# Kernel tuning notes

Measured on AMD Instinct MI355X. Metric: run time of the kernel, lower is better.

## Reference

```python
import jax, jax.numpy as jnp
import numpy as np

B, W, I, S, T, U, US = 4, 2000, 64, 64, 24, 32, 2
V, H, D, OUT = 32000, 4, 256, 512
PER = W + I + S + U + 1          # nodes per graph = 2161
N = B * PER                      # 8644 nodes
E_RAND = N * 16


def setup_inputs() -> dict:
    key = jax.random.key(0)
    ks = jax.random.split(key, 24)
    s = 0.02
    inp = {}
    inp["all_words"] = jax.random.randint(ks[0], (B * W,), 0, V)
    inp["image_feats"] = jax.random.normal(ks[1], (B * I, 2048), jnp.float32)
    inp["sentences"] = jax.random.randint(ks[2], (B, S, T), 0, V)
    inp["sentence_mask"] = jnp.ones((B, S, T), jnp.float32)
    inp["utterances"] = jax.random.randint(ks[3], (B, U, US), 0, S)
    inp["utterance_mask"] = jnp.ones((B, U, US), jnp.float32)
    inp["session_ids"] = (jnp.arange(B) + 1) * PER - 1   # last node of each graph
    src = jax.random.randint(ks[4], (E_RAND,), 0, N)
    dst = jax.random.randint(ks[5], (E_RAND,), 0, N)
    loop = jnp.arange(N)
    inp["edge_src"] = jnp.concatenate([src, loop])
    inp["edge_dst"] = jnp.concatenate([dst, loop])
    # learned parameters
    inp["word_embed"] = jax.random.normal(ks[6], (V, 300), jnp.float32) * s
    inp["text_fc_w"] = jax.random.normal(ks[7], (300, 1024), jnp.float32) * s
    inp["text_fc_b"] = jnp.zeros((1024,), jnp.float32)
    inp["image_fc_w"] = jax.random.normal(ks[8], (2048, 1024), jnp.float32) * s
    inp["image_fc_b"] = jnp.zeros((1024,), jnp.float32)
    inp["gat0_fc"] = jax.random.normal(ks[9], (1024, H * D), jnp.float32) * s
    inp["gat0_al"] = jax.random.normal(ks[10], (H, D), jnp.float32) * s
    inp["gat0_ar"] = jax.random.normal(ks[11], (H, D), jnp.float32) * s
    inp["gat0_b"] = jnp.zeros((H * D,), jnp.float32)
    inp["gat1_fc"] = jax.random.normal(ks[12], (H * D, H * D), jnp.float32) * s
    inp["gat1_al"] = jax.random.normal(ks[13], (H, D), jnp.float32) * s
    inp["gat1_ar"] = jax.random.normal(ks[14], (H, D), jnp.float32) * s
    inp["gat1_b"] = jnp.zeros((H * D,), jnp.float32)
    inp["gat2_fc"] = jax.random.normal(ks[15], (H * D, OUT), jnp.float32) * s
    inp["gat2_al"] = jax.random.normal(ks[16], (1, OUT), jnp.float32) * s
    inp["gat2_ar"] = jax.random.normal(ks[17], (1, OUT), jnp.float32) * s
    inp["gat2_b"] = jnp.zeros((OUT,), jnp.float32)
    return inp


def _gat_layer(h, src, dst, fc_w, al, ar, b, act):
    # DGL GATConv: fc -> per-head attention logits -> edge softmax over dst -> aggregate
    n = h.shape[0]
    nh, dd = al.shape
    f = (h @ fc_w).reshape(n, nh, dd)                    # [N,H,D]
    el = (f * al).sum(-1)                                # [N,H]
    er = (f * ar).sum(-1)
    e = jax.nn.leaky_relu(el[src] + er[dst], 0.2)        # [E,H]
    m = jax.ops.segment_max(e, dst, num_segments=n)      # stable softmax per dst node
    a = jnp.exp(e - m[dst])
    z = jax.ops.segment_sum(a, dst, num_segments=n)
    alpha = a / z[dst]                                   # [E,H]
    out = jax.ops.segment_sum(alpha[:, :, None] * f[src], dst, num_segments=n)
    out = out + b.reshape(nh, dd)
    if act:
        out = jax.nn.elu(out)
    return out.reshape(n, nh * dd)


def _masked_mean(x, mask):
    # x: [..., K, F], mask: [..., K]
    s = (x * mask[..., None]).sum(-2)
    cnt = mask.sum(-1, keepdims=True)
    cnt = jnp.where(cnt == 0, 1.0, cnt)
    return s / cnt


def reference(all_words, image_feats, sentences, sentence_mask, utterances,
              utterance_mask, session_ids, edge_src, edge_dst,
              word_embed, text_fc_w, text_fc_b, image_fc_w, image_fc_b,
              gat0_fc, gat0_al, gat0_ar, gat0_b,
              gat1_fc, gat1_al, gat1_ar, gat1_b,
              gat2_fc, gat2_al, gat2_ar, gat2_b):
    b, s_num, t_num = sentences.shape
    u_num, us_num = utterances.shape[1], utterances.shape[2]
    w_per = all_words.shape[0] // b
    i_per = image_feats.shape[0] // b

    # word nodes
    we = word_embed[all_words].reshape(b, w_per, 300)
    # sentence nodes: masked mean over words
    sw = word_embed[sentences]                           # [B,S,T,300]
    sent = _masked_mean(sw, sentence_mask)               # [B,S,300]
    # utterance nodes: gather sentence embeds, masked mean over sentences
    uidx = utterances.reshape(b, u_num * us_num)
    ue = jnp.take_along_axis(sent, uidx[:, :, None], axis=1).reshape(b, u_num, us_num, -1)
    utt = _masked_mean(ue, utterance_mask)               # [B,U,300]
    # session node
    sess = utt.mean(axis=1, keepdims=True)               # [B,1,300]

    txt = lambda x: x @ text_fc_w + text_fc_b
    wf, sf, uf, ssf = txt(we), txt(sent), txt(utt), txt(sess)
    imf = (image_feats @ image_fc_w + image_fc_b).reshape(b, i_per, -1)

    # node layout per graph: [words, images, sentences, utterances, session]
    h = jnp.concatenate([wf, imf, sf, uf, ssf], axis=1).reshape(-1, 1024)

    h = _gat_layer(h, edge_src, edge_dst, gat0_fc, gat0_al, gat0_ar, gat0_b, act=True)
    h = _gat_layer(h, edge_src, edge_dst, gat1_fc, gat1_al, gat1_ar, gat1_b, act=True)
    h = _gat_layer(h, edge_src, edge_dst, gat2_fc, gat2_al, gat2_ar, gat2_b, act=False)

    return h[session_ids]                                # [B, 512]
```

## Files before the change

kernel.cpp:

```cpp
#include <hip/hip_runtime.h>
#include <math.h>

constexpr int kB = 4, kW = 2000, kI = 64, kS = 64, kT = 24, kU = 32, kUS = 2;
constexpr int kPER = kW + kI + kS + kU + 1;
constexpr int kN   = kB * kPER;
constexpr int kTxtPer  = kW + kS + kU + 1;
constexpr int kTxtRows = kB * kTxtPer;
constexpr int kEmb = 300;
constexpr int kEmbPad = 320;
constexpr int kHid = 1024;
constexpr int kOut = 512;
constexpr int kCap = 256;
constexpr int kMaxDeg = 256;
constexpr int kNcB = 1152;

typedef __attribute__((ext_vector_type(8))) short bf16x8;
typedef __attribute__((ext_vector_type(4))) float f32x4;

__device__ __forceinline__ unsigned short f2bf(float f) {
  union { float f; unsigned int u; } x; x.f = f;
  unsigned int r = x.u + 0x7FFF + ((x.u >> 16) & 1);
  return (unsigned short)(r >> 16);
}
__device__ __forceinline__ float bf2f(unsigned short u) {
  union { unsigned int u; float f; } x; x.u = ((unsigned int)u) << 16;
  return x.f;
}

__device__ __forceinline__ void gl16(const unsigned short* g, unsigned short* l) {
  __builtin_amdgcn_global_load_lds(
      (const __attribute__((address_space(1))) void*)g,
      (__attribute__((address_space(3))) void*)l,
      16, 0, 0);
}

__global__ __launch_bounds__(256) void k_prep0(
    const float* __restrict__ tx_w, unsigned short* __restrict__ o_tx,
    const float* __restrict__ im_w, unsigned short* __restrict__ o_im,
    const float* __restrict__ g0_w, unsigned short* __restrict__ o_g0,
    const float* __restrict__ g1_w, unsigned short* __restrict__ o_g1,
    const float* __restrict__ g2_w, unsigned short* __restrict__ o_g2,
    const float* __restrict__ img, unsigned short* __restrict__ o_img,
    const int* __restrict__ sents, const float* __restrict__ smask,
    const float* __restrict__ wemb, float* __restrict__ sent,
    int* __restrict__ rmt, int* __restrict__ rmi,
    int* __restrict__ cnt, float* __restrict__ Cimg, float* __restrict__ Cg2) {
  int b = blockIdx.x;
  int tid = threadIdx.x;
  int tx = tid & 31, ty = tid >> 5;

  const float* in = nullptr; unsigned short* out = nullptr; int K = 0, N = 0, Kpad = 0, nbx = 0;
  if (b < 320)                { in = tx_w; out = o_tx; K = kEmb; N = kHid; Kpad = kEmbPad; nbx = 32; }
  else if ((b -= 320) < 2048) { in = im_w; out = o_im; K = 2048; N = kHid; Kpad = 2048; nbx = 32; }
  else if ((b -= 2048) < 1024){ in = g0_w; out = o_g0; K = kHid; N = kHid; Kpad = kHid; nbx = 32; }
  else if ((b -= 1024) < 1024){ in = g1_w; out = o_g1; K = kHid; N = kHid; Kpad = kHid; nbx = 32; }
  else if ((b -= 1024) < 512) { in = g2_w; out = o_g2; K = kHid; N = kOut; Kpad = kHid; nbx = 16; }
  else if ((b -= 512) < 512) {
    int i = b * 1024 + tid * 4;
    float4 v = *(const float4*)(img + i);
    ushort4 o; o.x = f2bf(v.x); o.y = f2bf(v.y); o.z = f2bf(v.z); o.w = f2bf(v.w);
    *(ushort4*)(o_img + i) = o;
    return;
  } else if ((b -= 512) < 256) {
    __shared__ int idx[kT];
    __shared__ float mk[kT];
    __shared__ float s_cnt;
    if (tid < kT) { idx[tid] = sents[b * kT + tid]; mk[tid] = smask[b * kT + tid]; }
    __syncthreads();
    if (tid == 0) {
      float c = 0.f;
      for (int i = 0; i < kT; ++i) c += mk[i];
      s_cnt = (c == 0.f) ? 1.f : c;
    }
    __syncthreads();
    for (int d = tid; d < kEmb; d += 256) {
      float acc = 0.f;
      for (int i = 0; i < kT; ++i) acc += wemb[idx[i] * kEmb + d] * mk[i];
      sent[b * kEmb + d] = acc / s_cnt;
    }
    return;
  } else if ((b -= 256) < 34) {
    int i = b * 256 + tid;
    if (i < kTxtRows) {
      int g = i / kTxtPer, j = i - g * kTxtPer;
      int base = g * kPER;
      int node;
      if (j < kW)                 node = base + j;
      else if (j < kW + kS)       node = base + kW + kI + (j - kW);
      else if (j < kW + kS + kU)  node = base + kW + kI + kS + (j - kW - kS);
      else                        node = base + kW + kI + kS + kU;
      rmt[i] = node;
    }
    if (i < kB * kI) {
      int g = i >> 6;
      rmi[i] = g * kPER + kW + (i & 63);
    }
    return;
  } else if ((b -= 34) < 34) {
    int i = b * 256 + tid;
    if (i < kN) cnt[i] = 0;
    return;
  } else if ((b -= 34) < 256) {
    uint4 z = make_uint4(0u, 0u, 0u, 0u);
    ((uint4*)Cimg)[b * 256 + tid] = z;
    return;
  } else if ((b -= 256) < 128) {
    uint4 z = make_uint4(0u, 0u, 0u, 0u);
    ((uint4*)Cg2)[b * 256 + tid] = z;
    return;
  } else {
    b -= 128;
    int i = b * 256 + tid;
    uint4 z = make_uint4(0u, 0u, 0u, 0u);
    ((uint4*)(o_g0 + (size_t)1032 * kHid))[i] = z;
    ((uint4*)(o_g1 + (size_t)1032 * kHid))[i] = z;
    return;
  }

  int bx = b % nbx, by = b / nbx;
  __shared__ float t[32][33];
  int n = bx * 32 + tx;
#pragma unroll
  for (int j = 0; j < 4; ++j) {
    int k = by * 32 + ty + j * 8;
    t[ty + j * 8][tx] = (k < K) ? in[(size_t)k * N + n] : 0.f;
  }
  __syncthreads();
#pragma unroll
  for (int j = 0; j < 4; ++j) {
    int nn = bx * 32 + ty + j * 8;
    int kk = by * 32 + tx;
    out[(size_t)nn * Kpad + kk] = f2bf(t[tx][ty + j * 8]);
  }
}

__global__ __launch_bounds__(256) void k_utt_sess(const int* __restrict__ utts,
                                                  const float* __restrict__ umask,
                                                  const float* __restrict__ sent,
                                                  float* __restrict__ utt,
                                                  float* __restrict__ sess,
                                                  const float* __restrict__ g0_w,
                                                  const float* __restrict__ g1_w,
                                                  const float* __restrict__ g0_al,
                                                  const float* __restrict__ g0_ar,
                                                  const float* __restrict__ g1_al,
                                                  const float* __restrict__ g1_ar,
                                                  unsigned short* __restrict__ o_g0,
                                                  unsigned short* __restrict__ o_g1) {
  int blk = blockIdx.x;
  int tid = threadIdx.x;
  if (blk < kB * kU) {
    int bu = blk, b = bu / kU;
    __shared__ int idx[kUS];
    __shared__ float mk[kUS];
    __shared__ float s_cnt;
    if (tid < kUS) { idx[tid] = utts[bu * kUS + tid]; mk[tid] = umask[bu * kUS + tid]; }
    __syncthreads();
    if (tid == 0) {
      float c = 0.f;
      for (int i = 0; i < kUS; ++i) c += mk[i];
      s_cnt = (c == 0.f) ? 1.f : c;
    }
    __syncthreads();
    for (int d = tid; d < kEmb; d += 256) {
      float acc = 0.f;
      for (int i = 0; i < kUS; ++i) acc += sent[(b * kS + idx[i]) * kEmb + d] * mk[i];
      utt[bu * kEmb + d] = acc / s_cnt;
    }
  } else if (blk < kB * kU + kB) {
    int b = blk - kB * kU;
    for (int d = tid; d < kEmb; d += 256) {
      float acc = 0.f;
      for (int u = 0; u < kU; ++u) {
        float ua = 0.f, c = 0.f;
        for (int us = 0; us < kUS; ++us) {
          int i = (b * kU + u) * kUS + us;
          int sidx = utts[i];
          float m = umask[i];
          ua += sent[(b * kS + sidx) * kEmb + d] * m;
          c += m;
        }
        if (c == 0.f) c = 1.f;
        acc += ua / c;
      }
      sess[b * kEmb + d] = acc * (1.f / kU);
    }
  } else {
    int b = blk - (kB * kU + kB);
    int layer = b >> 7, rem = b & 127;
    int which = rem >> 6;
    int rem2 = rem & 63;
    int h = rem2 >> 4, kblk = rem2 & 15;
    const float* fc = layer ? g1_w : g0_w;
    const float* a  = layer ? (which ? g1_ar : g1_al) : (which ? g0_ar : g0_al);
    unsigned short* wt = layer ? o_g1 : o_g0;
    int kl = tid >> 2, q = tid & 3;
    int k = kblk * 64 + kl;
    float s = 0.f;
    const float* fr = fc + (size_t)k * kHid + h * 256 + q * 64;
    const float* av = a + h * 256 + q * 64;
    for (int d = 0; d < 64; ++d) s += fr[d] * av[d];
    s += __shfl_xor(s, 1);
    s += __shfl_xor(s, 2);
    if (q == 0) wt[(size_t)(1024 + which * 4 + h) * kHid + k] = f2bf(s);
  }
}

__global__ __launch_bounds__(256) void k_txtcount(const int* __restrict__ aw,
                                                  const float* __restrict__ wemb,
                                                  const float* __restrict__ sent,
                                                  const float* __restrict__ utt,
                                                  const float* __restrict__ sess,
                                                  unsigned short* __restrict__ txt,
                                                  const int* __restrict__ dst,
                                                  int* __restrict__ cnt, int E) {
  int blk = blockIdx.x;
  int tid = threadIdx.x;
  if (blk < kTxtRows) {
    int r = blk;
    int g = r / kTxtPer, j = r - g * kTxtPer;
    const float* src;
    if (j < kW)                 src = wemb + (size_t)aw[g * kW + j] * kEmb;
    else if (j < kW + kS)       src = sent + (size_t)(g * kS + (j - kW)) * kEmb;
    else if (j < kW + kS + kU)  src = utt  + (size_t)(g * kU + (j - kW - kS)) * kEmb;
    else                        src = sess + (size_t)g * kEmb;
    for (int d = tid; d < kEmbPad; d += 256)
      txt[(size_t)r * kEmbPad + d] = (d < kEmb) ? f2bf(src[d]) : (unsigned short)0;
  } else {
    int e = (blk - kTxtRows) * 256 + tid;
    if (e < E) atomicAdd(&cnt[dst[e]], 1);
  }
}

template <bool OBF, bool ELR>
__global__ __launch_bounds__(256) void k_mm2(const unsigned short* __restrict__ A,
                                             const unsigned short* __restrict__ Bt,
                                             const float* __restrict__ bias,
                                             const int* __restrict__ rmap,
                                             void* __restrict__ Cout,
                                             float* __restrict__ el,
                                             float* __restrict__ er,
                                             int M, int K, int NcB, int NcOut) {
  __shared__ __align__(16) unsigned short As[128 * 64];
  __shared__ __align__(16) unsigned short Bs[128 * 64];
  int nCol = NcB >> 7;
  int bi = blockIdx.x;
  int xcd = bi & 7, bj = bi >> 3;
  int colTile = bj % nCol;
  int rowTile = ((bj / nCol) << 3) + xcd;
  int row0 = rowTile << 7;
  if (row0 >= M) return;
  int col0 = colTile << 7;

  int tid = threadIdx.x;
  int wid = tid >> 6, lane = tid & 63, quad = lane >> 4, l16 = lane & 15;
  int wm = wid >> 1, wn = wid & 1;

  f32x4 acc[4][4];
  f32x4 zero4 = {0.f, 0.f, 0.f, 0.f};
#pragma unroll
  for (int i = 0; i < 4; ++i)
#pragma unroll
    for (int j = 0; j < 4; ++j) acc[i][j] = zero4;

  int lr = lane >> 3;
  int swc = (lane & 7) ^ lr;

  for (int k0 = 0; k0 < K; k0 += 64) {
    __syncthreads();
#pragma unroll
    for (int i = 0; i < 4; ++i) {
      int rb = i * 32 + wid * 8;
      int r = rb + lr;
      int grow = row0 + r;
      if (grow >= M) grow = row0;
      gl16(A + (size_t)grow * K + k0 + (swc << 3), &As[rb * 64]);
      int nrow = col0 + r;
      gl16(Bt + (size_t)nrow * K + k0 + (swc << 3), &Bs[rb * 64]);
    }
    __syncthreads();
#pragma unroll
    for (int s = 0; s < 2; ++s) {
      int cc = s * 4 + quad;
      bf16x8 aF[4], bF[4];
#pragma unroll
      for (int mi = 0; mi < 4; ++mi) {
        int r = wm * 64 + mi * 16 + l16;
        aF[mi] = *(const bf16x8*)&As[r * 64 + ((cc ^ (r & 7)) << 3)];
      }
#pragma unroll
      for (int ni = 0; ni < 4; ++ni) {
        int r = wn * 64 + ni * 16 + l16;
        bF[ni] = *(const bf16x8*)&Bs[r * 64 + ((cc ^ (r & 7)) << 3)];
      }
#pragma unroll
      for (int mi = 0; mi < 4; ++mi)
#pragma unroll
        for (int ni = 0; ni < 4; ++ni)
          acc[mi][ni] = __builtin_amdgcn_mfma_f32_16x16x32_bf16(aF[mi], bF[ni], acc[mi][ni], 0, 0, 0);
    }
  }

#pragma unroll
  for (int mi = 0; mi < 4; ++mi) {
#pragma unroll
    for (int ni = 0; ni < 4; ++ni) {
      int gm0 = row0 + wm * 64 + mi * 16 + quad * 4;
      int gn  = col0 + wn * 64 + ni * 16 + l16;
      float bv = (bias && gn < NcOut) ? bias[gn] : 0.f;
#pragma unroll
      for (int i = 0; i < 4; ++i) {
        int r = gm0 + i;
        if (r >= M) continue;
        float v = acc[mi][ni][i] + bv;
        if (gn < NcOut) {
          if (OBF) {
            int orow = rmap ? rmap[r] : r;
            ((unsigned short*)Cout)[(size_t)orow * NcOut + gn] = f2bf(v);
          } else {
            ((float*)Cout)[(size_t)r * NcOut + gn] = v;
          }
        } else if (ELR) {
          int gn2 = gn - NcOut;
          if (gn2 < 4)      el[r * 4 + gn2] = v;
          else if (gn2 < 8) er[r * 4 + gn2 - 4] = v;
        }
      }
    }
  }
}

__global__ __launch_bounds__(256) void k_mm_sk(const unsigned short* __restrict__ A,
                                               const unsigned short* __restrict__ Bt,
                                               const int* __restrict__ rowlist,
                                               float* __restrict__ C,
                                               int M, int K, int Nc, int Kc) {
  __shared__ __align__(16) unsigned short As[64 * 64];
  __shared__ __align__(16) unsigned short Bs[64 * 64];
  int tid = threadIdx.x;
  int wid = tid >> 6, lane = tid & 63, quad = lane >> 4, l16 = lane & 15;
  int row0 = blockIdx.y * 64, col0 = blockIdx.x * 64;
  int k0 = blockIdx.z * Kc;
  int k1 = k0 + Kc; if (k1 > K) k1 = K;

  f32x4 acc[4];
  f32x4 zero4 = {0.f, 0.f, 0.f, 0.f};
#pragma unroll
  for (int i = 0; i < 4; ++i) acc[i] = zero4;

  int lr = lane >> 3;
  int swc = (lane & 7) ^ lr;

  int arow[2];
#pragma unroll
  for (int i = 0; i < 2; ++i) {
    int grow = row0 + i * 32 + wid * 8 + lr;
    int ar = 0;
    if (grow < M) ar = rowlist ? rowlist[grow] : grow;
    arow[i] = ar;
  }

  for (int kk = k0; kk < k1; kk += 64) {
    __syncthreads();
#pragma unroll
    for (int i = 0; i < 2; ++i) {
      int rb = i * 32 + wid * 8;
      gl16(A + (size_t)arow[i] * K + kk + (swc << 3), &As[rb * 64]);
      int nrow = col0 + rb + lr;
      gl16(Bt + (size_t)nrow * K + kk + (swc << 3), &Bs[rb * 64]);
    }
    __syncthreads();
#pragma unroll
    for (int s = 0; s < 2; ++s) {
      int cc = s * 4 + quad;
      bf16x8 bF;
      {
        int r = wid * 16 + l16;
        bF = *(const bf16x8*)&Bs[r * 64 + ((cc ^ (r & 7)) << 3)];
      }
#pragma unroll
      for (int mi = 0; mi < 4; ++mi) {
        int r = mi * 16 + l16;
        bf16x8 aF = *(const bf16x8*)&As[r * 64 + ((cc ^ (r & 7)) << 3)];
        acc[mi] = __builtin_amdgcn_mfma_f32_16x16x32_bf16(aF, bF, acc[mi], 0, 0, 0);
      }
    }
  }
#pragma unroll
  for (int mi = 0; mi < 4; ++mi) {
#pragma unroll
    for (int i = 0; i < 4; ++i) {
      int r = row0 + mi * 16 + quad * 4 + i;
      int c = col0 + wid * 16 + l16;
      if (r < M) atomicAdd(&C[(size_t)r * Nc + c], acc[mi][i]);
    }
  }
}

__global__ void k_sk_epi(const float* __restrict__ Cw, const float* __restrict__ bias,
                         const int* __restrict__ rmap, unsigned short* __restrict__ out,
                         int M, int Nc) {
  int i = blockIdx.x * blockDim.x + threadIdx.x;
  if (i >= M * Nc) return;
  int r = i / Nc, c = i - r * Nc;
  out[(size_t)rmap[r] * Nc + c] = f2bf(Cw[i] + bias[c]);
}

__global__ void k_scan(int* __restrict__ deg, int* __restrict__ offs, int n) {
  __shared__ int part[1024];
  int tid = threadIdx.x;
  int per = (n + 1023) >> 10;
  int start = tid * per;
  int local = 0;
  for (int i = 0; i < per; ++i) { int idx = start + i; if (idx < n) local += deg[idx]; }
  part[tid] = local;
  __syncthreads();
  for (int off = 1; off < 1024; off <<= 1) {
    int add = (tid >= off) ? part[tid - off] : 0;
    __syncthreads();
    part[tid] += add;
    __syncthreads();
  }
  int run = (tid == 0) ? 0 : part[tid - 1];
  for (int i = 0; i < per; ++i) {
    int idx = start + i;
    if (idx < n) { offs[idx] = run; run += deg[idx]; }
  }
  if (tid == 1023) offs[n] = part[1023];
  __syncthreads();
  for (int i = tid; i < n; i += 1024) deg[i] = 0;
}

__global__ void k_fill(const int* __restrict__ src, const int* __restrict__ dst,
                       const int* __restrict__ offs, int* __restrict__ cur,
                       int* __restrict__ csr, int E) {
  int e = blockIdx.x * blockDim.x + threadIdx.x;
  if (e < E) {
    int d = dst[e];
    int slot = offs[d] + atomicAdd(&cur[d], 1);
    csr[slot] = src[e];
  }
}

__global__ __launch_bounds__(256) void k_agg3(const unsigned short* __restrict__ f,
                                              const float* __restrict__ el,
                                              const float* __restrict__ er,
                                              const int* __restrict__ offs,
                                              const int* __restrict__ csr,
                                              const float* __restrict__ bias,
                                              unsigned short* __restrict__ out) {
  __shared__ float xs[4][kMaxDeg];
  int v = blockIdx.x;
  int tid = threadIdx.x;
  int h = tid >> 6, lane = tid & 63;
  int e0 = offs[v];
  int deg = offs[v + 1] - e0;
  if (deg > kMaxDeg) deg = kMaxDeg;

  float erv = er[v * 4 + h];
  float m = -1e30f;
  for (int base = 0; base < deg; base += 64) {
    int idx = base + lane;
    float x = -1e30f;
    if (idx < deg) {
      int s = csr[e0 + idx];
      x = el[s * 4 + h] + erv;
      x = x > 0.f ? x : 0.2f * x;
      xs[h][idx] = x;
    }
    float mm = x;
#pragma unroll
    for (int o = 32; o; o >>= 1) mm = fmaxf(mm, __shfl_xor(mm, o));
    m = fmaxf(m, mm);
  }
  float zs = 0.f;
  for (int base = 0; base < deg; base += 64) {
    int idx = base + lane;
    if (idx < deg) {
      float w = expf(xs[h][idx] - m);
      xs[h][idx] = w;
      zs += w;
    }
  }
#pragma unroll
  for (int o = 32; o; o >>= 1) zs += __shfl_xor(zs, o);
  float rz = 1.f / zs;
  for (int base = 0; base < deg; base += 64) {
    int idx = base + lane;
    if (idx < deg) xs[h][idx] *= rz;
  }
  __syncthreads();

  int d0 = tid * 4;
  float a0 = 0.f, a1 = 0.f, a2 = 0.f, a3 = 0.f;
  for (int e = 0; e < deg; ++e) {
    int s = csr[e0 + e];
    float w = xs[h][e];
    ushort4 fv = *(const ushort4*)(f + (size_t)s * 1024 + d0);
    a0 += w * bf2f(fv.x);
    a1 += w * bf2f(fv.y);
    a2 += w * bf2f(fv.z);
    a3 += w * bf2f(fv.w);
  }
  float4 bv = *(const float4*)(bias + d0);
  float o0 = a0 + bv.x, o1 = a1 + bv.y, o2 = a2 + bv.z, o3 = a3 + bv.w;
  o0 = o0 > 0.f ? o0 : expm1f(o0);
  o1 = o1 > 0.f ? o1 : expm1f(o1);
  o2 = o2 > 0.f ? o2 : expm1f(o2);
  o3 = o3 > 0.f ? o3 : expm1f(o3);
  ushort4 ov;
  ov.x = f2bf(o0); ov.y = f2bf(o1); ov.z = f2bf(o2); ov.w = f2bf(o3);
  *(ushort4*)(out + (size_t)v * 1024 + d0) = ov;
}

__global__ void k_rows2(const int* __restrict__ sid, const int* __restrict__ offs,
                        const int* __restrict__ csr, int* __restrict__ rowlist,
                        int* __restrict__ info) {
  __shared__ int degs[kB], starts[kB], total;
  int tid = threadIdx.x;
  int bv = tid >> 6, lane = tid & 63;
  if (tid < kB) {
    int v = sid[tid];
    degs[tid] = offs[v + 1] - offs[v];
  }
  __syncthreads();
  if (tid == 0) {
    int p = 0;
    for (int b = 0; b < kB; ++b) {
      starts[b] = p;
      int d = degs[b];
      if (p + d > kCap) d = kCap - p;
      degs[b] = d;
      p += d;
    }
    total = p;
  }
  __syncthreads();
  int v = sid[bv];
  int e0 = offs[v];
  int deg = degs[bv];
  int start = starts[bv];
  if (lane == 0) {
    info[bv] = start;
    info[4 + bv] = deg;
    info[8 + bv] = start;
  }
  __syncthreads();
  for (int idx = lane; idx < deg; idx += 64) {
    int s = csr[e0 + idx];
    rowlist[start + idx] = s;
    if (s == v) info[8 + bv] = start + idx;
  }
  for (int i = total + tid; i < kCap; i += 256) rowlist[i] = 0;
}

__global__ void k_elr_c(const float* __restrict__ fc, const float* __restrict__ al,
                        const float* __restrict__ ar, float* __restrict__ el,
                        float* __restrict__ er) {
  int r = blockIdx.x;
  int lane = threadIdx.x;
  float a = 0.f, b = 0.f;
  for (int d = lane * 4; d < 512; d += 256) {
    float4 x = *(const float4*)(fc + (size_t)r * 512 + d);
    float4 av = *(const float4*)(al + d);
    float4 rv = *(const float4*)(ar + d);
    a += x.x * av.x + x.y * av.y + x.z * av.z + x.w * av.w;
    b += x.x * rv.x + x.y * rv.y + x.z * rv.z + x.w * rv.w;
  }
#pragma unroll
  for (int off = 32; off; off >>= 1) {
    a += __shfl_down(a, off);
    b += __shfl_down(b, off);
  }
  if (lane == 0) { el[r] = a; er[r] = b; }
}

__global__ __launch_bounds__(256) void k_agg_fin2(const float* __restrict__ fc,
                                                  const float* __restrict__ el,
                                                  const float* __restrict__ er,
                                                  const int* __restrict__ info,
                                                  const float* __restrict__ bias,
                                                  float* __restrict__ out) {
  int bv = blockIdx.x;
  int tid = threadIdx.x;
  int start = info[bv], cnt = info[4 + bv];
  float erv = er[info[8 + bv]];
  float m = -1e30f;
  for (int i = 0; i < cnt; ++i) {
    float x = el[start + i] + erv;
    x = x > 0.f ? x : 0.2f * x;
    m = fmaxf(m, x);
  }
  float z = 0.f, a0 = 0.f, a1 = 0.f;
  for (int i = 0; i < cnt; ++i) {
    int r = start + i;
    float x = el[r] + erv;
    x = x > 0.f ? x : 0.2f * x;
    float w = expf(x - m);
    z += w;
    a0 += w * fc[(size_t)r * 512 + tid];
    a1 += w * fc[(size_t)r * 512 + 256 + tid];
  }
  out[bv * 512 + tid] = a0 / z + bias[tid];
  out[bv * 512 + 256 + tid] = a1 / z + bias[256 + tid];
}

extern "C" void kernel_launch(void* const* d_in, const int* in_sizes, int n_in,
                              void* d_out, int out_size, void* d_ws, size_t ws_size,
                              hipStream_t stream) {
  const int*   all_words   = (const int*)d_in[0];
  const float* image_feats = (const float*)d_in[1];
  const int*   sentences   = (const int*)d_in[2];
  const float* sent_mask   = (const float*)d_in[3];
  const int*   utterances  = (const int*)d_in[4];
  const float* utt_mask    = (const float*)d_in[5];
  const int*   session_ids = (const int*)d_in[6];
  const int*   edge_src    = (const int*)d_in[7];
  const int*   edge_dst    = (const int*)d_in[8];
  const float* word_embed  = (const float*)d_in[9];
  const float* text_fc_w   = (const float*)d_in[10];
  const float* text_fc_b   = (const float*)d_in[11];
  const float* image_fc_w  = (const float*)d_in[12];
  const float* image_fc_b  = (const float*)d_in[13];
  const float* gat0_fc     = (const float*)d_in[14];
  const float* gat0_al     = (const float*)d_in[15];
  const float* gat0_ar     = (const float*)d_in[16];
  const float* gat0_b      = (const float*)d_in[17];
  const float* gat1_fc     = (const float*)d_in[18];
  const float* gat1_al     = (const float*)d_in[19];
  const float* gat1_ar     = (const float*)d_in[20];
  const float* gat1_b      = (const float*)d_in[21];
  const float* gat2_fc     = (const float*)d_in[22];
  const float* gat2_al     = (const float*)d_in[23];
  const float* gat2_ar     = (const float*)d_in[24];
  const float* gat2_b      = (const float*)d_in[25];

  const int E = in_sizes[7];

  char* base = (char*)d_ws;
  size_t off = 0;
  auto alloc = [&](size_t elems, size_t esz) -> void* {
    void* p = base + off;
    off += ((elems * esz + 255) / 256) * 256;
    return p;
  };
  unsigned short* Abf   = (unsigned short*)alloc((size_t)kN * kHid, 2);
  unsigned short* fbf   = (unsigned short*)alloc((size_t)kN * kHid, 2);
  unsigned short* txtbf = (unsigned short*)alloc((size_t)kTxtRows * kEmbPad, 2);
  unsigned short* imgbf = (unsigned short*)alloc((size_t)kB * kI * 2048, 2);
  unsigned short* wtTx  = (unsigned short*)alloc((size_t)kHid * kEmbPad, 2);
  unsigned short* wtIm  = (unsigned short*)alloc((size_t)kHid * 2048, 2);
  unsigned short* wtG0  = (unsigned short*)alloc((size_t)kNcB * kHid, 2);
  unsigned short* wtG1  = (unsigned short*)alloc((size_t)kNcB * kHid, 2);
  unsigned short* wtG2  = (unsigned short*)alloc((size_t)kOut * kHid, 2);
  float* Cimg   = (float*)alloc((size_t)kB * kI * kHid, 4);
  float* Cg2    = (float*)alloc((size_t)kCap * kOut, 4);
  float* sentb  = (float*)alloc((size_t)kB * kS * kEmb, 4);
  float* uttb   = (float*)alloc((size_t)kB * kU * kEmb, 4);
  float* sessb  = (float*)alloc((size_t)kB * kEmb, 4);
  float* el     = (float*)alloc((size_t)kN * 4, 4);
  float* er     = (float*)alloc((size_t)kN * 4, 4);
  int*   offs   = (int*)alloc(kN + 1, 4);
  int*   cnt    = (int*)alloc(kN, 4);
  int*   csr    = (int*)alloc(E, 4);
  int*   rmt    = (int*)alloc(kTxtRows, 4);
  int*   rmi    = (int*)alloc(kB * kI, 4);
  int*   rowl   = (int*)alloc(kCap, 4);
  int*   info   = (int*)alloc(16, 4);
  (void)ws_size; (void)n_in; (void)out_size;

  constexpr int kPrepBlocks = 320 + 2048 + 1024 + 1024 + 512 + 512 + 256 + 34 + 34 + 256 + 128 + 60;
  k_prep0<<<kPrepBlocks, 256, 0, stream>>>(
      text_fc_w, wtTx, image_fc_w, wtIm, gat0_fc, wtG0, gat1_fc, wtG1, gat2_fc, wtG2,
      image_feats, imgbf, sentences, sent_mask, word_embed, sentb, rmt, rmi,
      cnt, Cimg, Cg2);

  k_utt_sess<<<kB * kU + kB + 256, 256, 0, stream>>>(
      utterances, utt_mask, sentb, uttb, sessb,
      gat0_fc, gat1_fc, gat0_al, gat0_ar, gat1_al, gat1_ar, wtG0, wtG1);

  k_txtcount<<<kTxtRows + (E + 255) / 256, 256, 0, stream>>>(
      all_words, word_embed, sentb, uttb, sessb, txtbf, edge_dst, cnt, E);

  k_scan<<<1, 1024, 0, stream>>>(cnt, offs, kN);
  k_fill<<<(E + 255) / 256, 256, 0, stream>>>(edge_src, edge_dst, offs, cnt, csr, E);

  auto mmGrid = [](int M, int NcB_) {
    int nrt = (M + 127) / 128;
    return 8 * (NcB_ / 128) * ((nrt + 7) / 8);
  };

  k_mm2<true, false><<<mmGrid(kTxtRows, kHid), 256, 0, stream>>>(
      txtbf, wtTx, text_fc_b, rmt, Abf, nullptr, nullptr, kTxtRows, kEmbPad, kHid, kHid);

  k_mm_sk<<<dim3(kHid / 64, kB * kI / 64, 4), 256, 0, stream>>>(
      imgbf, wtIm, nullptr, Cimg, kB * kI, 2048, kHid, 512);
  k_sk_epi<<<(kB * kI * kHid + 255) / 256, 256, 0, stream>>>(
      Cimg, image_fc_b, rmi, Abf, kB * kI, kHid);

  k_mm2<true, true><<<mmGrid(kN, kNcB), 256, 0, stream>>>(
      Abf, wtG0, nullptr, nullptr, fbf, el, er, kN, kHid, kNcB, kHid);
  k_agg3<<<kN, 256, 0, stream>>>(fbf, el, er, offs, csr, gat0_b, Abf);

  k_mm2<true, true><<<mmGrid(kN, kNcB), 256, 0, stream>>>(
      Abf, wtG1, nullptr, nullptr, fbf, el, er, kN, kHid, kNcB, kHid);
  k_agg3<<<kN, 256, 0, stream>>>(fbf, el, er, offs, csr, gat1_b, Abf);

  k_rows2<<<1, 256, 0, stream>>>(session_ids, offs, csr, rowl, info);
  k_mm_sk<<<dim3(kOut / 64, kCap / 64, 4), 256, 0, stream>>>(
      Abf, wtG2, rowl, Cg2, kCap, kHid, kOut, 256);
  k_elr_c<<<kCap, 64, 0, stream>>>(Cg2, gat2_al, gat2_ar, el, er);
  k_agg_fin2<<<kB, 256, 0, stream>>>(Cg2, el, er, info, gat2_b, (float*)d_out);
}
```

Before: 418.7 us.

## Remap GAT aggregation blocks to head-per-XCD groups with wave-per-node gathering

The aggregation kernel changes from one node per block (four heads across four waves) to one head per block, with each wave handling a different node. Blocks are mapped so that each XCD always processes the same head, which keeps that head's 256-column feature slice resident in the XCD's L2. Each wave gathers 16-byte vectors, with its two half-waves taking alternate edges and combining through a shuffle. The softmax normalisation is folded into the gather. The design relies on the round-robin assignment of blocks to XCDs and changes the order of the floating-point summation.

```diff
diff --git a/kernel.cpp b/kernel.cpp
--- a/kernel.cpp
+++ b/kernel.cpp
@@ -13,6 +13,8 @@
 constexpr int kCap = 256;
 constexpr int kMaxDeg = 256;
 constexpr int kNcB = 1152;
+constexpr int kNB  = kN / 4;
+constexpr int kNBhi = (kNB + 1) / 2;
 
 typedef __attribute__((ext_vector_type(8))) short bf16x8;
 typedef __attribute__((ext_vector_type(4))) float f32x4;
@@ -25,6 +27,12 @@
 __device__ __forceinline__ float bf2f(unsigned short u) {
   union { unsigned int u; float f; } x; x.u = ((unsigned int)u) << 16;
   return x.f;
+}
+__device__ __forceinline__ float bflo(unsigned int u) {
+  union { unsigned int u; float f; } x; x.u = u << 16; return x.f;
+}
+__device__ __forceinline__ float bfhi(unsigned int u) {
+  union { unsigned int u; float f; } x; x.u = u & 0xFFFF0000u; return x.f;
 }
 
 __device__ __forceinline__ void gl16(const unsigned short* g, unsigned short* l) {
@@ -442,31 +450,37 @@
   }
 }
 
-__global__ __launch_bounds__(256) void k_agg3(const unsigned short* __restrict__ f,
-                                              const float* __restrict__ el,
-                                              const float* __restrict__ er,
-                                              const int* __restrict__ offs,
-                                              const int* __restrict__ csr,
-                                              const float* __restrict__ bias,
-                                              unsigned short* __restrict__ out) {
+__global__ __launch_bounds__(256) void k_agg3h(const unsigned short* __restrict__ f,
+                                               const float* __restrict__ el,
+                                               const float* __restrict__ er,
+                                               const int* __restrict__ offs,
+                                               const int* __restrict__ csr,
+                                               const float* __restrict__ bias,
+                                               unsigned short* __restrict__ out) {
   __shared__ float xs[4][kMaxDeg];
-  int v = blockIdx.x;
-  int tid = threadIdx.x;
-  int h = tid >> 6, lane = tid & 63;
+  int bid = blockIdx.x;
+  int xcd = bid & 7;
+  int g = xcd & 3;
+  int nb = (xcd >> 2) * kNBhi + (bid >> 3);
+  if (nb >= kNB) return;
+  int tid = threadIdx.x;
+  int wid = tid >> 6, lane = tid & 63;
+  int v = nb * 4 + wid;
+
   int e0 = offs[v];
   int deg = offs[v + 1] - e0;
   if (deg > kMaxDeg) deg = kMaxDeg;
 
-  float erv = er[v * 4 + h];
+  float erv = er[v * 4 + g];
   float m = -1e30f;
   for (int base = 0; base < deg; base += 64) {
     int idx = base + lane;
     float x = -1e30f;
     if (idx < deg) {
       int s = csr[e0 + idx];
-      x = el[s * 4 + h] + erv;
+      x = el[s * 4 + g] + erv;
       x = x > 0.f ? x : 0.2f * x;
-      xs[h][idx] = x;
+      xs[wid][idx] = x;
     }
     float mm = x;
 #pragma unroll
@@ -477,40 +491,56 @@
   for (int base = 0; base < deg; base += 64) {
     int idx = base + lane;
     if (idx < deg) {
-      float w = expf(xs[h][idx] - m);
-      xs[h][idx] = w;
+      float w = expf(xs[wid][idx] - m);
+      xs[wid][idx] = w;
       zs += w;
     }
   }
 #pragma unroll
   for (int o = 32; o; o >>= 1) zs += __shfl_xor(zs, o);
   float rz = 1.f / zs;
-  for (int base = 0; base < deg; base += 64) {
-    int idx = base + lane;
-    if (idx < deg) xs[h][idx] *= rz;
-  }
-  __syncthreads();
-
-  int d0 = tid * 4;
+
+  int side = lane >> 5, l32 = lane & 31;
+  int d0 = g * 256 + l32 * 8;
   float a0 = 0.f, a1 = 0.f, a2 = 0.f, a3 = 0.f;
-  for (int e = 0; e < deg; ++e) {
-    int s = csr[e0 + e];
-    float w = xs[h][e];
-    ushort4 fv = *(const ushort4*)(f + (size_t)s * 1024 + d0);
-    a0 += w * bf2f(fv.x);
-    a1 += w * bf2f(fv.y);
-    a2 += w * bf2f(fv.z);
-    a3 += w * bf2f(fv.w);
-  }
-  float4 bv = *(const float4*)(bias + d0);
-  float o0 = a0 + bv.x, o1 = a1 + bv.y, o2 = a2 + bv.z, o3 = a3 + bv.w;
-  o0 = o0 > 0.f ? o0 : expm1f(o0);
-  o1 = o1 > 0.f ? o1 : expm1f(o1);
-  o2 = o2 > 0.f ? o2 : expm1f(o2);
-  o3 = o3 > 0.f ? o3 : expm1f(o3);
-  ushort4 ov;
-  ov.x = f2bf(o0); ov.y = f2bf(o1); ov.z = f2bf(o2); ov.w = f2bf(o3);
-  *(ushort4*)(out + (size_t)v * 1024 + d0) = ov;
+  float a4 = 0.f, a5 = 0.f, a6 = 0.f, a7 = 0.f;
+  for (int e = 0; e < deg; e += 2) {
+    int idx = e + side;
+    if (idx < deg) {
+      float w = xs[wid][idx] * rz;
+      int s = csr[e0 + idx];
+      uint4 fv = *(const uint4*)(f + (size_t)s * 1024 + d0);
+      a0 += w * bflo(fv.x); a1 += w * bfhi(fv.x);
+      a2 += w * bflo(fv.y); a3 += w * bfhi(fv.y);
+      a4 += w * bflo(fv.z); a5 += w * bfhi(fv.z);
+      a6 += w * bflo(fv.w); a7 += w * bfhi(fv.w);
+    }
+  }
+  a0 += __shfl_xor(a0, 32); a1 += __shfl_xor(a1, 32);
+  a2 += __shfl_xor(a2, 32); a3 += __shfl_xor(a3, 32);
+  a4 += __shfl_xor(a4, 32); a5 += __shfl_xor(a5, 32);
+  a6 += __shfl_xor(a6, 32); a7 += __shfl_xor(a7, 32);
+
+  if (side == 0) {
+    float4 b0 = *(const float4*)(bias + d0);
+    float4 b1 = *(const float4*)(bias + d0 + 4);
+    float o0 = a0 + b0.x, o1 = a1 + b0.y, o2 = a2 + b0.z, o3 = a3 + b0.w;
+    float o4 = a4 + b1.x, o5 = a5 + b1.y, o6 = a6 + b1.z, o7 = a7 + b1.w;
+    o0 = o0 > 0.f ? o0 : expm1f(o0);
+    o1 = o1 > 0.f ? o1 : expm1f(o1);
+    o2 = o2 > 0.f ? o2 : expm1f(o2);
+    o3 = o3 > 0.f ? o3 : expm1f(o3);
+    o4 = o4 > 0.f ? o4 : expm1f(o4);
+    o5 = o5 > 0.f ? o5 : expm1f(o5);
+    o6 = o6 > 0.f ? o6 : expm1f(o6);
+    o7 = o7 > 0.f ? o7 : expm1f(o7);
+    uint4 ov;
+    ov.x = (unsigned)f2bf(o0) | ((unsigned)f2bf(o1) << 16);
+    ov.y = (unsigned)f2bf(o2) | ((unsigned)f2bf(o3) << 16);
+    ov.z = (unsigned)f2bf(o4) | ((unsigned)f2bf(o5) << 16);
+    ov.w = (unsigned)f2bf(o6) | ((unsigned)f2bf(o7) << 16);
+    *(uint4*)(out + (size_t)v * 1024 + d0) = ov;
+  }
 }
 
 __global__ void k_rows2(const int* __restrict__ sid, const int* __restrict__ offs,
@@ -700,11 +730,11 @@
 
   k_mm2<true, true><<<mmGrid(kN, kNcB), 256, 0, stream>>>(
       Abf, wtG0, nullptr, nullptr, fbf, el, er, kN, kHid, kNcB, kHid);
-  k_agg3<<<kN, 256, 0, stream>>>(fbf, el, er, offs, csr, gat0_b, Abf);
+  k_agg3h<<<8 * kNBhi, 256, 0, stream>>>(fbf, el, er, offs, csr, gat0_b, Abf);
 
   k_mm2<true, true><<<mmGrid(kN, kNcB), 256, 0, stream>>>(
       Abf, wtG1, nullptr, nullptr, fbf, el, er, kN, kHid, kNcB, kHid);
-  k_agg3<<<kN, 256, 0, stream>>>(fbf, el, er, offs, csr, gat1_b, Abf);
+  k_agg3h<<<8 * kNBhi, 256, 0, stream>>>(fbf, el, er, offs, csr, gat1_b, Abf);
 
   k_rows2<<<1, 256, 0, stream>>>(session_ids, offs, csr, rowl, info);
   k_mm_sk<<<dim3(kOut / 64, kCap / 64, 4), 256, 0, stream>>>(
```

Measured after the change: 433.0 us. 3.4% more time.
